# Kernel tuning notes

Hardware: AMD Instinct MI355X
Metric: run time of the kernel (lower is better)

## Reference

```python
import jax, jax.numpy as jnp
import numpy as np

IOU_THRESHOLDS = (0.5, 0.75)
B, N, G = 256, 4000, 50


def _iou(amin, amax, bmin, bmax):
    # broadcasted temporal IoU: anchors [N,1] vs boxes [1,G] -> [N,G]
    inter = jnp.maximum(jnp.minimum(amax, bmax) - jnp.maximum(amin, bmin), 0.0)
    union = (amax - amin) + (bmax - bmin) - inter
    return inter / union


def _greedy_tp(segments, gts, thr):
    # segments: [N,2], gts: [G,2]. Replicates AP.get_values greedy matching:
    # for each label (in order), claim the first (lowest-index) unused proposal
    # whose IoU > thr. Final used-mask == is_TP.
    ious = _iou(segments[:, 0:1], segments[:, 1:2], gts[None, :, 0], gts[None, :, 1])  # [N,G]
    pot = ious > thr
    n = segments.shape[0]

    def step(used, col):  # col: [N] bool, candidates for this label
        cand = col & ~used
        idx = jnp.argmax(cand)  # first True (argmax of bool is first max)
        used = jnp.where(jnp.any(cand), used.at[idx].set(True), used)
        return used, None

    used, _ = jax.lax.scan(step, jnp.zeros((n,), jnp.bool_), pot.T)
    return used  # [N] bool


def _ap_for_threshold(scores, segments, labels, thr):
    is_tp = jax.vmap(lambda s, g: _greedy_tp(s, g, thr))(segments, labels)  # [B,N]
    conf = scores.reshape(-1)                       # [B*N]
    tp = is_tp.reshape(-1).astype(jnp.float32)
    order = jnp.argsort(-conf)                      # sort by confidence, descending
    tp = tp[order]
    n_labels = labels.shape[0] * labels.shape[1]
    m = tp.shape[0]
    acc_tp = jnp.cumsum(tp)
    precision = acc_tp / (jnp.arange(m, dtype=jnp.float32) + 1.0)
    recall = acc_tp / jnp.float32(n_labels)
    # curve = [[1,0]] then (recall, precision) reversed; AP = sum(|dx| * cummax(y)[:-1])
    x = jnp.concatenate([jnp.ones((1,), jnp.float32), recall[::-1]])
    y = jnp.concatenate([jnp.zeros((1,), jnp.float32), precision[::-1]])
    y_max = jax.lax.cummax(y, axis=0)
    x_diff = jnp.abs(jnp.diff(x))
    return jnp.sum(x_diff * y_max[:-1])


def setup_inputs() -> dict:
    key = jax.random.key(0)
    k1, k2, k3, k4, k5 = jax.random.split(key, 5)
    scores = jax.random.uniform(k1, (B, N), dtype=jnp.float32)
    p_start = jax.random.uniform(k2, (B, N), dtype=jnp.float32) * 0.9
    p_len = jax.random.uniform(k3, (B, N), dtype=jnp.float32) * 0.1 + 0.005
    segments = jnp.stack([p_start, p_start + p_len], axis=-1)  # [B,N,2], start<end
    g_start = jax.random.uniform(k4, (B, G), dtype=jnp.float32) * 0.9
    g_len = jax.random.uniform(k5, (B, G), dtype=jnp.float32) * 0.1 + 0.005
    labels = jnp.stack([g_start, g_start + g_len], axis=-1)    # [B,G,2]
    return {"scores": scores, "segments": segments, "labels": labels}


def reference(scores, segments, labels):
    # returns AP at each IoU threshold, shape [len(IOU_THRESHOLDS)]
    return jnp.stack([_ap_for_threshold(scores, segments, labels, t) for t in IOU_THRESHOLDS])
```

## Files before the change

### kernel.cpp

```cpp
#include <hip/hip_runtime.h>


#define B_ 256
#define N_ 4000
#define G_ 50
#define M_ (B_ * N_)
#define NL_ (B_ * G_)
#define NBKT 4096
#define SBKT 2048

typedef unsigned long long u64;

__device__ __forceinline__ unsigned bucket_of(float c) {
    unsigned b = (unsigned)(c * 4096.0f);
    return b > (NBKT - 1) ? (NBKT - 1) : b;
}

__global__ __launch_bounds__(1024) void tp_kernel(
    const float* __restrict__ seg,
    const float* __restrict__ gts,
    const float* __restrict__ conf,
    int* __restrict__ tpIdx,
    int* __restrict__ cnt,
    unsigned short* __restrict__ pbh)
{
    const int tid  = threadIdx.x;
    const int lane = tid & 63;
    const int wv   = tid >> 6;
    const int b    = blockIdx.x;

    __shared__ float2 gtl[G_];
    __shared__ u64 cand[2][G_][64];
    __shared__ unsigned hls[NBKT / 2];
    __shared__ int lcnt[2];

    #pragma unroll
    for (int k = 0; k < NBKT / 2048; ++k) hls[k * 1024 + tid] = 0u;
    if (tid < G_) gtl[tid] = ((const float2*)gts)[b * G_ + tid];
    if (tid < 2) lcnt[tid] = 0;
    __syncthreads();

    const float* cb = conf + (size_t)b * N_;
    #pragma unroll
    for (int s = 0; s < 4; ++s) {
        int n = s * 1024 + tid;
        if (n < N_) {
            unsigned bin = bucket_of(cb[n]);
            atomicAdd(&hls[bin >> 1], 1u << ((bin & 1) * 16));
        }
    }

    const float2* sb = (const float2*)(seg + (size_t)b * (N_ * 2));
    float pmin[4], pmax[4], plen[4];
    #pragma unroll
    for (int s = 0; s < 4; ++s) {
        int n = s * 1024 + tid;
        if (n < N_) { float2 v = sb[n]; pmin[s] = v.x; pmax[s] = v.y; }
        else { pmin[s] = 1e9f; pmax[s] = 1e9f; }
        plen[s] = pmax[s] - pmin[s];
    }
    for (int g = 0; g < G_; ++g) {
        float2 gt = gtl[g];
        float glen = gt.y - gt.x;
        u64 m0[4], m1[4];
        #pragma unroll
        for (int s = 0; s < 4; ++s) {
            float inter = fmaxf(fminf(pmax[s], gt.y) - fmaxf(pmin[s], gt.x), 0.0f);
            float uni = plen[s] + glen - inter;
            float e25 = uni * 0x1p-25f;
            float d   = inter - 0.5f * uni;
            m0[s] = __ballot(d > e25);
            m1[s] = __ballot((d - 0.25f * uni) > e25);
        }
        if (lane == 0) {
            #pragma unroll
            for (int s = 0; s < 4; ++s) {
                cand[0][g][s * 16 + wv] = m0[s];
                cand[1][g][s * 16 + wv] = m1[s];
            }
        }
    }
    __syncthreads();

    {
        unsigned* prow = (unsigned*)(pbh + (size_t)b * NBKT);
        #pragma unroll
        for (int k = 0; k < NBKT / 2048; ++k)
            prow[k * 1024 + tid] = hls[k * 1024 + tid];
    }

    if (wv < 2) {
        const int thr_i = wv;
        u64 used = 0ull;
        for (int g = 0; g < G_; ++g) {
            u64 c = cand[thr_i][g][lane] & ~used;
            u64 ball = __ballot(c != 0ull);
            if (ball) {
                int fl = __ffsll(ball) - 1;
                if (lane == fl) used |= (c & (0ull - c));
            }
        }
        int cpop = __popcll(used);
        if (cpop) {
            int j = atomicAdd(&lcnt[thr_i], cpop);
            u64 u = used;
            while (u) {
                int bit = __ffsll(u) - 1;
                u &= u - 1;
                tpIdx[thr_i * NL_ + b * G_ + j++] = b * N_ + lane * 64 + bit;
            }
        }
    }
    __syncthreads();
    if (tid < 2) cnt[tid * B_ + b] = lcnt[tid];
}

__global__ __launch_bounds__(256) void s1_kernel(
    unsigned short* __restrict__ pbh,
    unsigned* __restrict__ total)
{
    __shared__ unsigned short tile[256][32];
    __shared__ unsigned segsum[8][32];
    const int j = blockIdx.x;
    const int t = threadIdx.x;
    uint4* dst = (uint4*)&tile[t][0];
    const uint4* src = (const uint4*)(pbh + (size_t)t * NBKT + j * 32);
    #pragma unroll
    for (int k = 0; k < 4; ++k) dst[k] = src[k];
    __syncthreads();

    const int col = t & 31, seg = t >> 5;
    unsigned run = 0;
    #pragma unroll
    for (int i = 0; i < 32; ++i) run += tile[seg * 32 + i][col];
    segsum[seg][col] = run;
    __syncthreads();
    unsigned off0 = 0;
    #pragma unroll
    for (int s = 0; s < 8; ++s) off0 += (s < seg) ? segsum[s][col] : 0u;
    if (seg == 7) total[j * 32 + col] = off0 + segsum[7][col];
    unsigned run2 = off0;
    #pragma unroll
    for (int i = 0; i < 32; ++i) {
        unsigned v = tile[seg * 32 + i][col];
        tile[seg * 32 + i][col] = (unsigned short)run2;
        run2 += v;
    }
    __syncthreads();
    uint4* back = (uint4*)(pbh + (size_t)t * NBKT + j * 32);
    #pragma unroll
    for (int k = 0; k < 4; ++k) back[k] = dst[k];
}

__global__ __launch_bounds__(1024) void scatter_kernel(
    const float* __restrict__ conf,
    const unsigned short* __restrict__ pbh,
    const unsigned* __restrict__ total,
    unsigned* __restrict__ binStartG,
    u64* __restrict__ sKey)
{
    __shared__ unsigned baseB[NBKT];
    __shared__ unsigned lofs[NBKT];
    __shared__ unsigned wtot[16];
    const int tid = threadIdx.x;
    const int lane = tid & 63;
    const int wv = tid >> 6;
    const int b = blockIdx.x;

    uint4 v4 = ((const uint4*)total)[tid];
    unsigned own = v4.x + v4.y + v4.z + v4.w;
    unsigned inc = own;
    #pragma unroll
    for (int off = 1; off < 64; off <<= 1) {
        unsigned o = __shfl_up(inc, off, 64);
        if (lane >= off) inc += o;
    }
    if (lane == 63) wtot[wv] = inc;
    __syncthreads();
    if (wv == 0) {
        unsigned w = (lane < 16) ? wtot[lane] : 0u;
        unsigned wi = w;
        #pragma unroll
        for (int off = 1; off < 16; off <<= 1) {
            unsigned o = __shfl_up(wi, off, 64);
            if (lane >= off) wi += o;
        }
        if (lane < 16) wtot[lane] = wi - w;
    }
    __syncthreads();
    unsigned start = (inc - own) + wtot[wv];
    baseB[4 * tid]     = start;
    baseB[4 * tid + 1] = start + v4.x;
    baseB[4 * tid + 2] = start + v4.x + v4.y;
    baseB[4 * tid + 3] = start + v4.x + v4.y + v4.z;
    __syncthreads();
    #pragma unroll
    for (int k = 0; k < 4; ++k) {
        int bin = k * 1024 + tid;
        unsigned bs = baseB[bin];
        if (b == 0) binStartG[bin] = bs;
        baseB[bin] = bs + pbh[(size_t)b * NBKT + bin];
        lofs[bin] = 0u;
    }
    __syncthreads();

    const float* cb = conf + (size_t)b * N_;
    #pragma unroll
    for (int s4 = 0; s4 < 4; ++s4) {
        int n = s4 * 1024 + tid;
        if (n < N_) {
            float c = cb[n];
            unsigned bin = bucket_of(c);
            unsigned lo = atomicAdd(&lofs[bin], 1u);
            unsigned idx = (unsigned)(b * N_ + n);
            sKey[baseB[bin] + lo] = ((u64)__float_as_uint(c) << 32) | (u64)(0xFFFFFFFFu - idx);
        }
    }
}

__global__ __launch_bounds__(256) void rank_kernel(
    const float* __restrict__ conf,
    const int* __restrict__ tpIdx,
    const int* __restrict__ cnt,
    const unsigned* __restrict__ total,
    const unsigned* __restrict__ binStart,
    const u64* __restrict__ sKey,
    int* __restrict__ tpRank)
{
    const int lane = threadIdx.x & 63;
    const int w = (blockIdx.x << 2) | (threadIdx.x >> 6);
    if (w >= 2 * NL_) return;
    const int thr_i = w / NL_;
    const int t = w - thr_i * NL_;
    const int batch = t / G_;
    const int j = t - batch * G_;

    if (j < cnt[thr_i * B_ + batch]) {
        int e = tpIdx[thr_i * NL_ + t];
        float c = conf[e];
        u64 keyE = ((u64)__float_as_uint(c) << 32) | (u64)(0xFFFFFFFFu - (unsigned)e);
        unsigned bin = bucket_of(c);
        unsigned lo = binStart[bin], n = total[bin];
        int r = M_ - (int)lo - (int)n;
        for (unsigned base = 0; base < n; base += 64) {
            unsigned k = base + lane;
            bool pred = (k < n) && (sKey[lo + k] > keyE);
            r += (int)__popcll(__ballot(pred));
        }
        if (lane == 0) tpRank[thr_i * NL_ + t] = r;
    } else {
        if (lane == 0) tpRank[thr_i * NL_ + t] = M_ + t;
    }
}

__global__ __launch_bounds__(1024) void sortap_kernel(
    const int* __restrict__ tpRank,
    float* __restrict__ out)
{
    const int C = 13;
    union U1 { unsigned wtot[16]; float wmaxs[16]; };
    union U2 { unsigned hist[SBKT]; double red[1024]; };
    __shared__ int sr[NL_];
    __shared__ U1 u1;
    __shared__ U2 u2;
    const int thr_i = blockIdx.x;
    const int t = threadIdx.x;
    const int lane = t & 63;
    const int wv = t >> 6;

    u2.hist[t] = 0u; u2.hist[t + 1024] = 0u;
    __syncthreads();

    int r[C]; unsigned beta[C];
    #pragma unroll
    for (int k = 0; k < C; ++k) {
        int i = t + k * 1024;
        if (i < NL_) {
            int rr = tpRank[thr_i * NL_ + i];
            r[k] = rr;
            unsigned bb = ((unsigned)rr) >> 9;
            beta[k] = bb > (SBKT - 1) ? (SBKT - 1) : bb;
            atomicAdd(&u2.hist[beta[k]], 1u);
        } else { r[k] = 0; beta[k] = 0xFFFFFFFFu; }
    }
    __syncthreads();

    unsigned h0 = u2.hist[2 * t], h1 = u2.hist[2 * t + 1];
    unsigned own = h0 + h1;
    unsigned inc = own;
    #pragma unroll
    for (int off = 1; off < 64; off <<= 1) {
        unsigned o = __shfl_up(inc, off, 64);
        if (lane >= off) inc += o;
    }
    if (lane == 63) u1.wtot[wv] = inc;
    __syncthreads();
    if (wv == 0) {
        unsigned w = (lane < 16) ? u1.wtot[lane] : 0u;
        unsigned wi = w;
        #pragma unroll
        for (int off = 1; off < 16; off <<= 1) {
            unsigned o = __shfl_up(wi, off, 64);
            if (lane >= off) wi += o;
        }
        if (lane < 16) u1.wtot[lane] = wi - w;
    }
    __syncthreads();
    unsigned base = (inc - own) + u1.wtot[wv];
    __syncthreads();
    u2.hist[2 * t] = base;
    u2.hist[2 * t + 1] = base + h0;
    __syncthreads();

    #pragma unroll
    for (int k = 0; k < C; ++k)
        if (beta[k] != 0xFFFFFFFFu) {
            unsigned slot = atomicAdd(&u2.hist[beta[k]], 1u);
            sr[slot] = r[k];
        }
    __syncthreads();

    int p[C];
    #pragma unroll
    for (int k = 0; k < C; ++k) {
        if (beta[k] != 0xFFFFFFFFu) {
            unsigned st = (beta[k] == 0u) ? 0u : u2.hist[beta[k] - 1];
            unsigned en = u2.hist[beta[k]];
            int c = 0;
            for (unsigned j = st; j < en; ++j) c += (sr[j] < r[k]);
            p[k] = (int)st + c;
        } else p[k] = -1;
    }
    __syncthreads();
    #pragma unroll
    for (int k = 0; k < C; ++k)
        if (p[k] >= 0) sr[p[k]] = r[k];
    __syncthreads();

    float pr[C]; int rk[C];
    #pragma unroll
    for (int k = 0; k < C; ++k) {
        int i = t * C + k;
        rk[k] = (i < NL_) ? sr[i] : 0x7FFFFFFF;
        pr[k] = (rk[k] < M_) ? (float)(i + 1) / (float)(rk[k] + 1) : -1.0f;
    }
    float suf[C];
    float run = -1.0f;
    #pragma unroll
    for (int k = C - 1; k >= 0; --k) { run = fmaxf(run, pr[k]); suf[k] = run; }

    float m = run;
    #pragma unroll
    for (int off = 1; off < 64; off <<= 1) {
        float o = __shfl_down(m, off, 64);
        if (lane + off < 64) m = fmaxf(m, o);
    }
    float f_in = __shfl_down(m, 1, 64);
    if (lane == 63) f_in = -1.0f;
    if (lane == 0) u1.wmaxs[wv] = m;
    __syncthreads();
    if (wv == 0) {
        float wm = (lane < 16) ? u1.wmaxs[lane] : -1.0f;
        float mi = wm;
        #pragma unroll
        for (int off = 1; off < 16; off <<= 1) {
            float o = __shfl_down(mi, off, 64);
            if (lane + off < 64) mi = fmaxf(mi, o);
        }
        float fw = __shfl_down(mi, 1, 64);
        if (lane >= 15) fw = -1.0f;
        if (lane < 16) u1.wmaxs[lane] = fw;
    }
    __syncthreads();
    float follow = fmaxf(f_in, u1.wmaxs[wv]);

    double acc = 0.0;
    #pragma unroll
    for (int k = 0; k < C; ++k) {
        int i = t * C + k;
        if (rk[k] >= 1 && rk[k] < M_) {
            float smax = fmaxf(suf[k], follow);
            float rhi = (float)(i + 1) / 12800.0f;
            float rlo = (float)i / 12800.0f;
            acc += (double)((rhi - rlo) * smax);
        }
    }
    __syncthreads();
    u2.red[t] = acc;
    __syncthreads();
    for (int off = 512; off >= 1; off >>= 1) {
        if (t < off) u2.red[t] += u2.red[t + off];
        __syncthreads();
    }
    if (t == 0) out[thr_i] = (float)u2.red[0];
}

extern "C" void kernel_launch(void* const* d_in, const int* in_sizes, int n_in,
                              void* d_out, int out_size, void* d_ws, size_t ws_size,
                              hipStream_t stream) {
    const float* scores = (const float*)d_in[0];
    const float* seg    = (const float*)d_in[1];
    const float* gts    = (const float*)d_in[2];
    float* out = (float*)d_out;

    char* p = (char*)d_ws;
    int*            cnt        = (int*)p;             p += 4096;
    int*            tpIdx      = (int*)p;             p += 2 * NL_ * 4;
    int*            tpRank     = (int*)p;             p += 2 * NL_ * 4;
    unsigned*       total      = (unsigned*)p;        p += NBKT * 4;
    unsigned*       binStart   = (unsigned*)p;        p += NBKT * 4;
    unsigned short* pbh        = (unsigned short*)p;  p += (size_t)B_ * NBKT * 2;
    u64*            sKey       = (u64*)p;             p += (size_t)M_ * 8;
    (void)ws_size; (void)in_sizes; (void)n_in; (void)out_size;

    tp_kernel<<<B_, 1024, 0, stream>>>(seg, gts, scores, tpIdx, cnt, pbh);
    s1_kernel<<<NBKT / 32, 256, 0, stream>>>(pbh, total);
    scatter_kernel<<<B_, 1024, 0, stream>>>(scores, pbh, total, binStart, sKey);
    rank_kernel<<<(2 * NL_ + 3) / 4, 256, 0, stream>>>(scores, tpIdx, cnt,
                                                       total, binStart, sKey, tpRank);
    sortap_kernel<<<2, 1024, 0, stream>>>(tpRank, out);
}
```

Before: 159.0 us.

## Replace single-block bucket sort of TP ranks with parallel rank-counting kernels

The 2-block sortap kernel, which histogram-sorts 12800 TP ranks per threshold inside one workgroup, is split into three kernels. pos1 computes each element's position by counting smaller ranks across 16 tiles over a 13x16x2 grid. sumpr sums the partial counts and scatters precision and rank values to their sorted positions. apfin does the cummax and AP reduction. The aim is to spread the serial sort across many CUs, at the cost of O(n^2) comparisons, two extra launches, and reusing the sKey buffer as scratch for the partial counts.

```diff
diff --git a/kernel.cpp b/kernel.cpp
--- a/kernel.cpp
+++ b/kernel.cpp
@@ -7,7 +7,8 @@
 #define M_ (B_ * N_)
 #define NL_ (B_ * G_)
 #define NBKT 4096
-#define SBKT 2048
+#define KP 16
+#define TILE (NL_ / KP)
 
 typedef unsigned long long u64;
 
@@ -253,96 +254,76 @@
     }
 }
 
-__global__ __launch_bounds__(1024) void sortap_kernel(
+__global__ __launch_bounds__(256) void pos1_kernel(
     const int* __restrict__ tpRank,
+    int* __restrict__ pcount)
+{
+    __shared__ alignas(16) int tile[TILE];
+    const int k = blockIdx.y, thr_i = blockIdx.z;
+    const int* base = tpRank + thr_i * NL_;
+    for (int i = threadIdx.x; i < TILE; i += 256)
+        tile[i] = base[k * TILE + i];
+    __syncthreads();
+
+    const int t0 = blockIdx.x * 1024 + threadIdx.x;
+    int r[4], c[4] = {0, 0, 0, 0};
+    #pragma unroll
+    for (int j = 0; j < 4; ++j) {
+        int t = t0 + j * 256;
+        r[j] = (t < NL_) ? base[t] : -1;
+    }
+    const int4* l4 = (const int4*)tile;
+    #pragma unroll 4
+    for (int i = 0; i < TILE / 4; ++i) {
+        int4 v = l4[i];
+        #pragma unroll
+        for (int j = 0; j < 4; ++j)
+            c[j] += (v.x < r[j]) + (v.y < r[j]) + (v.z < r[j]) + (v.w < r[j]);
+    }
+    #pragma unroll
+    for (int j = 0; j < 4; ++j) {
+        int t = t0 + j * 256;
+        if (t < NL_) pcount[(thr_i * KP + k) * NL_ + t] = c[j];
+    }
+}
+
+__global__ __launch_bounds__(256) void sumpr_kernel(
+    const int* __restrict__ tpRank,
+    const int* __restrict__ pcount,
+    float* __restrict__ prA,
+    int* __restrict__ rkA)
+{
+    const int thr_i = blockIdx.y;
+    const int t = blockIdx.x * 256 + threadIdx.x;
+    int p = 0;
+    #pragma unroll
+    for (int k = 0; k < KP; ++k)
+        p += pcount[(thr_i * KP + k) * NL_ + t];
+    int r = tpRank[thr_i * NL_ + t];
+    float pr = (r < M_) ? (float)(p + 1) / (float)(r + 1) : -1.0f;
+    prA[thr_i * NL_ + p] = pr;
+    rkA[thr_i * NL_ + p] = r;
+}
+
+__global__ __launch_bounds__(1024) void apfin_kernel(
+    const float* __restrict__ prA,
+    const int* __restrict__ rkA,
     float* __restrict__ out)
 {
     const int C = 13;
-    union U1 { unsigned wtot[16]; float wmaxs[16]; };
-    union U2 { unsigned hist[SBKT]; double red[1024]; };
-    __shared__ int sr[NL_];
-    __shared__ U1 u1;
-    __shared__ U2 u2;
+    __shared__ double red[1024];
+    __shared__ float wmaxs[16];
     const int thr_i = blockIdx.x;
     const int t = threadIdx.x;
     const int lane = t & 63;
     const int wv = t >> 6;
 
-    u2.hist[t] = 0u; u2.hist[t + 1024] = 0u;
-    __syncthreads();
-
-    int r[C]; unsigned beta[C];
-    #pragma unroll
-    for (int k = 0; k < C; ++k) {
-        int i = t + k * 1024;
-        if (i < NL_) {
-            int rr = tpRank[thr_i * NL_ + i];
-            r[k] = rr;
-            unsigned bb = ((unsigned)rr) >> 9;
-            beta[k] = bb > (SBKT - 1) ? (SBKT - 1) : bb;
-            atomicAdd(&u2.hist[beta[k]], 1u);
-        } else { r[k] = 0; beta[k] = 0xFFFFFFFFu; }
-    }
-    __syncthreads();
-
-    unsigned h0 = u2.hist[2 * t], h1 = u2.hist[2 * t + 1];
-    unsigned own = h0 + h1;
-    unsigned inc = own;
-    #pragma unroll
-    for (int off = 1; off < 64; off <<= 1) {
-        unsigned o = __shfl_up(inc, off, 64);
-        if (lane >= off) inc += o;
-    }
-    if (lane == 63) u1.wtot[wv] = inc;
-    __syncthreads();
-    if (wv == 0) {
-        unsigned w = (lane < 16) ? u1.wtot[lane] : 0u;
-        unsigned wi = w;
-        #pragma unroll
-        for (int off = 1; off < 16; off <<= 1) {
-            unsigned o = __shfl_up(wi, off, 64);
-            if (lane >= off) wi += o;
-        }
-        if (lane < 16) u1.wtot[lane] = wi - w;
-    }
-    __syncthreads();
-    unsigned base = (inc - own) + u1.wtot[wv];
-    __syncthreads();
-    u2.hist[2 * t] = base;
-    u2.hist[2 * t + 1] = base + h0;
-    __syncthreads();
-
-    #pragma unroll
-    for (int k = 0; k < C; ++k)
-        if (beta[k] != 0xFFFFFFFFu) {
-            unsigned slot = atomicAdd(&u2.hist[beta[k]], 1u);
-            sr[slot] = r[k];
-        }
-    __syncthreads();
-
-    int p[C];
-    #pragma unroll
-    for (int k = 0; k < C; ++k) {
-        if (beta[k] != 0xFFFFFFFFu) {
-            unsigned st = (beta[k] == 0u) ? 0u : u2.hist[beta[k] - 1];
-            unsigned en = u2.hist[beta[k]];
-            int c = 0;
-            for (unsigned j = st; j < en; ++j) c += (sr[j] < r[k]);
-            p[k] = (int)st + c;
-        } else p[k] = -1;
-    }
-    __syncthreads();
-    #pragma unroll
-    for (int k = 0; k < C; ++k)
-        if (p[k] >= 0) sr[p[k]] = r[k];
-    __syncthreads();
-
     float pr[C]; int rk[C];
     #pragma unroll
     for (int k = 0; k < C; ++k) {
         int i = t * C + k;
-        rk[k] = (i < NL_) ? sr[i] : 0x7FFFFFFF;
-        pr[k] = (rk[k] < M_) ? (float)(i + 1) / (float)(rk[k] + 1) : -1.0f;
+        if (i < NL_) { pr[k] = prA[thr_i * NL_ + i]; rk[k] = rkA[thr_i * NL_ + i]; }
+        else { pr[k] = -1.0f; rk[k] = 0x7FFFFFFF; }
     }
     float suf[C];
     float run = -1.0f;
@@ -357,10 +338,10 @@
     }
     float f_in = __shfl_down(m, 1, 64);
     if (lane == 63) f_in = -1.0f;
-    if (lane == 0) u1.wmaxs[wv] = m;
+    if (lane == 0) wmaxs[wv] = m;
     __syncthreads();
     if (wv == 0) {
-        float wm = (lane < 16) ? u1.wmaxs[lane] : -1.0f;
+        float wm = (lane < 16) ? wmaxs[lane] : -1.0f;
         float mi = wm;
         #pragma unroll
         for (int off = 1; off < 16; off <<= 1) {
@@ -369,10 +350,10 @@
         }
         float fw = __shfl_down(mi, 1, 64);
         if (lane >= 15) fw = -1.0f;
-        if (lane < 16) u1.wmaxs[lane] = fw;
-    }
-    __syncthreads();
-    float follow = fmaxf(f_in, u1.wmaxs[wv]);
+        if (lane < 16) wmaxs[lane] = fw;
+    }
+    __syncthreads();
+    float follow = fmaxf(f_in, wmaxs[wv]);
 
     double acc = 0.0;
     #pragma unroll
@@ -385,14 +366,13 @@
             acc += (double)((rhi - rlo) * smax);
         }
     }
-    __syncthreads();
-    u2.red[t] = acc;
+    red[t] = acc;
     __syncthreads();
     for (int off = 512; off >= 1; off >>= 1) {
-        if (t < off) u2.red[t] += u2.red[t + off];
+        if (t < off) red[t] += red[t + off];
         __syncthreads();
     }
-    if (t == 0) out[thr_i] = (float)u2.red[0];
+    if (t == 0) out[thr_i] = (float)red[0];
 }
 
 extern "C" void kernel_launch(void* const* d_in, const int* in_sizes, int n_in,
@@ -411,6 +391,9 @@
     unsigned*       binStart   = (unsigned*)p;        p += NBKT * 4;
     unsigned short* pbh        = (unsigned short*)p;  p += (size_t)B_ * NBKT * 2;
     u64*            sKey       = (u64*)p;             p += (size_t)M_ * 8;
+    float*          prA        = (float*)p;           p += 2 * NL_ * 4;
+    int*            rkA        = (int*)p;             p += 2 * NL_ * 4;
+    int*            pcount     = (int*)sKey;
     (void)ws_size; (void)in_sizes; (void)n_in; (void)out_size;
 
     tp_kernel<<<B_, 1024, 0, stream>>>(seg, gts, scores, tpIdx, cnt, pbh);
@@ -418,5 +401,7 @@
     scatter_kernel<<<B_, 1024, 0, stream>>>(scores, pbh, total, binStart, sKey);
     rank_kernel<<<(2 * NL_ + 3) / 4, 256, 0, stream>>>(scores, tpIdx, cnt,
                                                        total, binStart, sKey, tpRank);
-    sortap_kernel<<<2, 1024, 0, stream>>>(tpRank, out);
-}
+    pos1_kernel<<<dim3(13, KP, 2), 256, 0, stream>>>(tpRank, pcount);
+    sumpr_kernel<<<dim3(50, 2), 256, 0, stream>>>(tpRank, pcount, prA, rkA);
+    apfin_kernel<<<2, 1024, 0, stream>>>(prA, rkA, out);
+}
```

Measured after the change: 173.3 us. 9.0% more time.
